# Optimization experiments

Hardware: AMD Instinct MI355X
Metric: run time of the kernel (lower is better)

The kernel has to match this reference:

```python
import jax, jax.numpy as jnp
import numpy as np

N, H, DK, DV, DFF, D = 2, 8, 32, 32, 512, 256
B, S = 2, 2048
MASK_VALUE = -1e-30
EPS = 1e-14  # K.epsilon()**2 with default epsilon 1e-7


def glorot(key, shape):
    fan_in, fan_out = shape[-2], shape[-1]
    limit = np.sqrt(6.0 / (fan_in + fan_out))
    return jax.random.uniform(key, shape, jnp.float32, -limit, limit)


def setup_inputs() -> dict:
    key = jax.random.key(0)
    ks = jax.random.split(key, 8)
    return {
        "x": jax.random.normal(ks[0], (B, S, D), jnp.float32),
        "mask": jnp.ones((B, S), jnp.float32),
        "Wq": glorot(ks[1], (N, H, D, DK)),
        "Wk": glorot(ks[2], (N, H, D, DK)),
        "Wv": glorot(ks[3], (N, H, D, DV)),
        "Wo": glorot(ks[4], (N, H * DV, D)),
        "W1": glorot(ks[5], (N, D, DFF)),
        "b1": jnp.zeros((N, DFF), jnp.float32),
        "W2": glorot(ks[6], (N, DFF, D)),
        "b2": jnp.zeros((N, D), jnp.float32),
        "gamma": jnp.ones((2 * N,), jnp.float32),
        "beta": jnp.zeros((2 * N,), jnp.float32),
    }


def _layernorm(x, g, b):
    mean = jnp.mean(x, axis=-1, keepdims=True)
    var = jnp.mean(jnp.square(x - mean), axis=-1, keepdims=True)
    return (x - mean) / jnp.sqrt(var + EPS) * g + b


def reference(x, mask, Wq, Wk, Wv, Wo, W1, b1, W2, b2, gamma, beta):
    m = mask[:, None, None, :]  # [B,1,1,S], multiplies score rows' key axis
    for i in range(N):
        # batched multi-head attention (no 1/sqrt(dk) scaling, faithful to source)
        q = jnp.einsum("bsd,hdk->bhsk", x, Wq[i])
        k = jnp.einsum("bsd,hdk->bhsk", x, Wk[i])
        v = jnp.einsum("bsd,hdv->bhsv", x, Wv[i])
        A = jnp.einsum("bhsk,bhtk->bhst", q, k)  # [B,H,S,S]
        A = m * A + (1.0 - m) * MASK_VALUE
        A = jax.nn.softmax(A, axis=-1)
        o = jnp.einsum("bhst,bhtv->bhsv", A, v)
        conc = o.transpose(0, 2, 1, 3).reshape(x.shape[0], x.shape[1], H * DV)
        x = x + conc @ Wo[i]
        x = _layernorm(x, gamma[2 * i], beta[2 * i])
        ffn = jax.nn.relu(x @ W1[i] + b1[i]) @ W2[i] + b2[i]
        x = x + ffn
        x = _layernorm(x, gamma[2 * i + 1], beta[2 * i + 1])
    return x
```

## Files before the change

kernel.cpp:

```cpp
#include <hip/hip_runtime.h>
#include <hip/hip_bf16.h>

#define NL 2
#define NH 8
#define DKk 32
#define DVv 32
#define DFF 512
#define DD 256
#define BB 2
#define SS 2048
#define MROWS (BB*SS)
#define LN_EPS 1e-14f
#define L2E 1.4426950408889634f
#define SOFT_SHIFT_L2E (50.0f*L2E)

typedef __hip_bfloat16 bf16;
typedef unsigned short us;
typedef short bf16x8 __attribute__((ext_vector_type(8)));
typedef float f32x4  __attribute__((ext_vector_type(4)));
typedef unsigned short us4 __attribute__((ext_vector_type(4)));

#define O_XF   256
#define O_QB   (O_XF+1048576)
#define O_KH   (O_QB+1048576)
#define O_KL   (O_KH+524288)
#define O_VT   (O_KL+524288)
#define O_XH   (O_VT+524288)
#define O_XL   (O_XH+524288)
#define O_OP   (O_XL+524288)
#define O_ML   (O_OP+2097152)
#define O_MASK (O_ML+65536)
#define O_B1   (O_MASK+4096)
#define O_B2   (O_B1+1024)
#define O_GM   (O_B2+512)
#define O_BT   (O_GM+4)
#define O_PREP (O_BT+4)
#define TAIL_TOTAL (4096+1024+512+4+4)
#define CONV_BLOCKS (512 + (TAIL_TOTAL+255)/256)
#define PREP_BLOCKS 512
#define PQH 0u
#define PQL 393216u
#define POH 786432u
#define POL 917504u
#define P1H 1048576u
#define P1L 1310720u
#define P2H 1572864u
#define P2L 1835008u

__device__ __forceinline__ float us2f(us u){
  unsigned int v = ((unsigned int)u) << 16; float f;
  __builtin_memcpy(&f, &v, 4); return f;
}
__device__ __forceinline__ us f2bf_rne(float f){
  unsigned int b = __float_as_uint(f);
  b += 0x7FFFu + ((b>>16)&1u);
  return (us)(b>>16);
}

#if __has_builtin(__builtin_amdgcn_exp2f)
#define EXP2F(x) __builtin_amdgcn_exp2f(x)
#else
#define EXP2F(x) exp2f(x)
#endif

#if __has_builtin(__builtin_amdgcn_cvt_pk_bf16_f32)
typedef __bf16 bf16x2_t __attribute__((ext_vector_type(2)));
__device__ __forceinline__ int pack_bf16(float a, float b){
  bf16x2_t r = __builtin_amdgcn_cvt_pk_bf16_f32(a, b);
  int i; __builtin_memcpy(&i, &r, 4); return i;
}
#else
__device__ __forceinline__ int pack_bf16(float a, float b){
  int b0 = __float_as_int(a) + 0x8000;
  int b1 = __float_as_int(b) + 0x8000;
  return (b1 & 0xFFFF0000) | ((int)((unsigned)b0 >> 16));
}
#endif

__device__ __forceinline__ f32x4 MF(bf16x8 a, bf16x8 b, f32x4 c){
  return __builtin_amdgcn_mfma_f32_16x16x32_bf16(a,b,c,0,0,0);
}

__device__ __forceinline__ void gl_lds16(const us* g, us* l){
  __builtin_amdgcn_global_load_lds(
    (const __attribute__((address_space(1))) unsigned int*)g,
    (__attribute__((address_space(3))) unsigned int*)l, 16, 0, 0);
}

__device__ __forceinline__ size_t xhl_idx(int row, int col){
  int rt = row>>6, rg = (row>>4)&3, L15 = row&15;
  int kc = col>>5, Q = (col>>3)&3, j = col&7;
  return ((size_t)(rt*8+kc))*2048 + rg*512 + Q*128 + L15*8 + j;
}

__device__ __forceinline__ float conv1(const void* src, size_t i, int flag){
  if(flag) return ((const float*)src)[i];
  return us2f(((const us*)src)[i]);
}

__device__ __forceinline__ void prep_b_raw(const void* W0, const void* W1v, const void* W2v,
                                           int baseoff, us* __restrict__ Bh, us* __restrict__ Bl,
                                           int Kd, int Nd, int qkv, int g, int flag)
{
  int total = (Kd/32)*(Nd/16)*64;
  if(g >= total) return;
  int lane = g & 63, fi = g >> 6;
  int ncN = Nd/16;
  int nc = fi % ncN, kc = fi / ncN;
  int Q = lane>>4, L15 = lane&15;
  int n = nc*16 + L15;
  const void* src;
  int off0, stride;
  if(qkv){
    int sec = n>>8, h = (n>>5)&7, kq = n&31;
    src = (sec==0)?W0:((sec==1)?W1v:W2v);
    off0 = baseoff + h*8192 + kq;
    stride = 32;
  } else {
    src = W0;
    off0 = baseoff + n;
    stride = Nd;
  }
  #pragma unroll
  for(int j=0;j<8;j++){
    int k = kc*32 + Q*8 + j;
    float v = conv1(src, (size_t)off0 + (size_t)k*stride, flag);
    us hb = f2bf_rne(v);
    Bh[(size_t)g*8 + j] = hb;
    Bl[(size_t)g*8 + j] = f2bf_rne(v - us2f(hb));
  }
}

__global__ void conv_prep(const void* s0, const void* s1, const void* sWq, const void* sWk,
                          const void* sWv, const void* sWo, const void* sW1, const void* sb1,
                          const void* sW2, const void* sb2, const void* sgm, const void* sbt,
                          float* __restrict__ ws, int* __restrict__ flagp)
{
  __shared__ int fsh[4];
  int bad = 0;
  const us* xr = (const us*)s0;
  for(int i=threadIdx.x; i<4096; i+=256){
    float f = us2f(xr[i]);
    if(!(fabsf(f) < 1e3f)) bad = 1;
  }
  unsigned long long m = __ballot(bad);
  if((threadIdx.x&63)==0) fsh[threadIdx.x>>6] = (m!=0ull);
  __syncthreads();
  int flag = (fsh[0]|fsh[1]|fsh[2]|fsh[3]);
  if(blockIdx.x==0 && threadIdx.x==0) *flagp = flag;

  int b = blockIdx.x;
  if(b < PREP_BLOCKS){
    int layer = b >> 8, lb = b & 255;
    us* prep = (us*)(ws + O_PREP);
    if(lb < 96){
      int g = lb*256 + threadIdx.x;
      prep_b_raw(sWq, sWk, sWv, layer*65536, prep+PQH+(size_t)layer*196608,
                 prep+PQL+(size_t)layer*196608, 256, 768, 1, g, flag);
    } else if(lb < 128){
      int g = (lb-96)*256 + threadIdx.x;
      prep_b_raw(sWo, nullptr, nullptr, layer*65536, prep+POH+(size_t)layer*65536,
                 prep+POL+(size_t)layer*65536, 256, 256, 0, g, flag);
    } else if(lb < 192){
      int g = (lb-128)*256 + threadIdx.x;
      prep_b_raw(sW1, nullptr, nullptr, layer*131072, prep+P1H+(size_t)layer*131072,
                 prep+P1L+(size_t)layer*131072, 256, 512, 0, g, flag);
    } else {
      int g = (lb-192)*256 + threadIdx.x;
      prep_b_raw(sW2, nullptr, nullptr, layer*131072, prep+P2H+(size_t)layer*131072,
                 prep+P2L+(size_t)layer*131072, 512, 256, 0, g, flag);
    }
    return;
  }
  int b2 = b - PREP_BLOCKS;
  if(b2 < 512){
    int g8 = b2*256 + threadIdx.x;
    int e0 = g8*8;
    float v[8];
    if(flag){
      float4 a0 = *((const float4*)s0 + (e0>>2));
      float4 a1 = *((const float4*)s0 + (e0>>2) + 1);
      v[0]=a0.x; v[1]=a0.y; v[2]=a0.z; v[3]=a0.w;
      v[4]=a1.x; v[5]=a1.y; v[6]=a1.z; v[7]=a1.w;
    } else {
      bf16x8 u = *((const bf16x8*)s0 + g8);
      #pragma unroll
      for(int j=0;j<8;j++) v[j] = us2f((us)u[j]);
    }
    *(float4*)&ws[O_XF+e0]   = (float4){v[0],v[1],v[2],v[3]};
    *(float4*)&ws[O_XF+e0+4] = (float4){v[4],v[5],v[6],v[7]};
    union{ us a[8]; uint4 q; } hh, ll;
    #pragma unroll
    for(int j=0;j<8;j++){
      us hb = f2bf_rne(v[j]);
      hh.a[j] = hb;
      ll.a[j] = f2bf_rne(v[j] - us2f(hb));
    }
    size_t xi = xhl_idx(e0>>8, e0&255);
    *(uint4*)&((us*)(ws+O_XH))[xi] = hh.q;
    *(uint4*)&((us*)(ws+O_XL))[xi] = ll.q;
    return;
  }
  int g = (b2-512)*256 + threadIdx.x;
  if(g < 4096){ ws[O_MASK+g] = conv1(s1, g, flag)*L2E; return; }
  g -= 4096;
  if(g < 1024){ ws[O_B1+g] = conv1(sb1, g, flag); return; }
  g -= 1024;
  if(g < 512){ ws[O_B2+g] = conv1(sb2, g, flag); return; }
  g -= 512;
  if(g < 4){ ws[O_GM+g] = conv1(sgm, g, flag); return; }
  g -= 4;
  if(g < 4){ ws[O_BT+g] = conv1(sbt, g, flag); return; }
}

template<int MODE>
__launch_bounds__(256)
__global__ void gemm_mfma(const us* __restrict__ Axh, const us* __restrict__ Axl,
                          const us* __restrict__ Bh, const us* __restrict__ Bl,
                          const float* __restrict__ bias,
                          float* __restrict__ O,
                          us* __restrict__ QH, us* __restrict__ QL,
                          us* __restrict__ KH, us* __restrict__ KL, us* __restrict__ VT,
                          int Ncols, int Kdim)
{
  __shared__ __align__(16) us SH[16384];
  const int t = threadIdx.x;
  const int w = t>>6, lane = t&63;
  const int Q = lane>>4, L15 = lane&15;
  const int bx = blockIdx.x, by = blockIdx.y;
  const int row0 = bx*64;
  const int nc0 = by*4;
  const int col0 = by*64;
  const int nKc = Kdim>>5;
  const int ncW = Ncols>>4;

  f32x4 acc[2][2];
  #pragma unroll
  for(int i=0;i<2;i++)
    #pragma unroll
    for(int j=0;j<2;j++) acc[i][j] = (f32x4){0.f,0.f,0.f,0.f};

  auto stage = [&](int kc){
    const int bo = (kc&1)*8192;
    size_t abase = ((size_t)(bx*nKc + kc))*2048;
    gl_lds16(&Axh[abase + (size_t)t*8], &SH[bo + t*8]);
    gl_lds16(&Axl[abase + (size_t)t*8], &SH[bo + 2048 + t*8]);
    size_t gidx = ((size_t)(kc*ncW + nc0 + w)*64 + lane)*8;
    gl_lds16(&Bh[gidx], &SH[bo + 4096 + t*8]);
    gl_lds16(&Bl[gidx], &SH[bo + 6144 + t*8]);
  };

  stage(0);

  for(int kc=0; kc<nKc; kc++){
    __syncthreads();
    if(kc+1 < nKc) stage(kc+1);
    const int bo = (kc&1)*8192;
    const us* Ah  = SH + bo;
    const us* Al  = SH + bo + 2048;
    const us* Bhs = SH + bo + 4096;
    const us* Bls = SH + bo + 6144;

    bf16x8 aAh[2], aAl[2], bBh[2], bBl[2];
    #pragma unroll
    for(int rg2=0;rg2<2;rg2++){
      int rg = (w&1)*2 + rg2;
      aAh[rg2] = *(const bf16x8*)&Ah[rg*512 + lane*8];
      aAl[rg2] = *(const bf16x8*)&Al[rg*512 + lane*8];
    }
    #pragma unroll
    for(int cg2=0;cg2<2;cg2++){
      int nc = (w>>1)*2 + cg2;
      bBh[cg2] = *(const bf16x8*)&Bhs[nc*512 + lane*8];
      bBl[cg2] = *(const bf16x8*)&Bls[nc*512 + lane*8];
    }
    #pragma unroll
    for(int rg2=0;rg2<2;rg2++)
      #pragma unroll
      for(int cg2=0;cg2<2;cg2++){
        acc[rg2][cg2] = MF(aAl[rg2], bBh[cg2], acc[rg2][cg2]);
        acc[rg2][cg2] = MF(aAh[rg2], bBl[cg2], acc[rg2][cg2]);
        acc[rg2][cg2] = MF(aAh[rg2], bBh[cg2], acc[rg2][cg2]);
      }
  }

  if(MODE==0){
    __syncthreads();
    us* TH = SH;
    us* TL = SH + 4608;
    #pragma unroll
    for(int rg2=0;rg2<2;rg2++)
      #pragma unroll
      for(int cg2=0;cg2<2;cg2++)
        #pragma unroll
        for(int r=0;r<4;r++){
          int rl = (w&1)*32 + rg2*16 + Q*4 + r;
          int cl = (w>>1)*32 + cg2*16 + L15;
          float va = acc[rg2][cg2][r];
          us hb = f2bf_rne(va);
          TH[rl*72+cl] = hb;
          TL[rl*72+cl] = f2bf_rne(va - us2f(hb));
        }
    __syncthreads();
    const int sec = col0>>8;
    const int h0  = (col0&255)>>5;
    const int b_  = row0>>11;
    const int srow0 = row0 & 2047;
    if(sec < 2){
      us* DH = (sec==0) ? QH : KH;
      us* DL = (sec==0) ? QL : KL;
      #pragma unroll
      for(int u2=0; u2<2; u2++){
        int u = w + u2*4;
        int rg = u&3, half = u>>2;
        int lbase = (rg*16 + L15)*72 + half*32 + Q*8;
        bf16x8 hv = *(const bf16x8*)&TH[lbase];
        bf16x8 lv = *(const bf16x8*)&TL[lbase];
        int bh = b_*NH + h0 + half;
        size_t dbase = ((size_t)(bh*128 + (srow0>>4) + rg)*64 + lane)*8;
        *(bf16x8*)&DH[dbase] = hv;
        *(bf16x8*)&DL[dbase] = lv;
      }
    } else {
      #pragma unroll
      for(int u2=0; u2<2; u2++){
        int u = w + u2*4;
        int sgrp = u&1, kqh = (u>>1)&1, half = u>>2;
        union{ us u8[8]; bf16x8 v; } vv;
        #pragma unroll
        for(int j=0;j<8;j++){
          int rl = sgrp*32 + Q*8 + j;
          int cl = half*32 + kqh*16 + L15;
          vv.u8[j] = TH[rl*72+cl];
        }
        int bh = b_*NH + h0 + half;
        size_t dbase = ((size_t)((bh*64 + (srow0>>5) + sgrp)*2 + kqh)*64 + lane)*8;
        *(bf16x8*)&VT[dbase] = vv.v;
      }
    }
  } else {
    #pragma unroll
    for(int rg2=0;rg2<2;rg2++)
      #pragma unroll
      for(int cg2=0;cg2<2;cg2++)
        #pragma unroll
        for(int r=0;r<4;r++){
          int row = row0 + (w&1)*32 + rg2*16 + Q*4 + r;
          int c   = col0 + (w>>1)*32 + cg2*16 + L15;
          float v = acc[rg2][cg2][r] + bias[c];
          O[(size_t)row*Ncols + c] = v>0.f ? v : 0.f;
        }
  }
}

__launch_bounds__(512)
__global__ void oln_ffn(const float* __restrict__ OpartA, const float* __restrict__ MLA,
                        const us* __restrict__ WOh, const us* __restrict__ WOl,
                        const us* __restrict__ W1h, const us* __restrict__ W1l,
                        const us* __restrict__ W2h, const us* __restrict__ W2l,
                        const float* __restrict__ b1, const float* __restrict__ b2,
                        float* __restrict__ xf, us* __restrict__ xh, us* __restrict__ xl,
                        const float* __restrict__ gamma, const float* __restrict__ beta, int gi0,
                        void* __restrict__ out, int write_out, const int* __restrict__ flagp)
{
  __shared__ __align__(16) us xAH[4096], xAL[4096];
  __shared__ __align__(16) us hAH[8192], hAL[8192];
  __shared__ float lred[256];
  const int t = threadIdx.x;
  const int w = t>>6, lane = t&63;
  const int Q = lane>>4, L15 = lane&15;
  const int row0 = blockIdx.x*16;
  const int b_ = row0>>11, s0_ = row0&2047;

  bf16x8 Wh[4][2], Wl[4][2];
  float4 Ar[2][4];
  float  Ml[2][2];

  auto loadWO_ = [&](int kc, int set){
    #pragma unroll
    for(int cg=0;cg<2;cg++){
      size_t fi = (size_t)(kc*16 + w*2 + cg)*512 + (size_t)lane*8;
      Wh[set][cg] = *(const bf16x8*)&WOh[fi];
      Wl[set][cg] = *(const bf16x8*)&WOl[fi];
    }
  };
  auto loadW1_ = [&](int nch, int kc, int set){
    #pragma unroll
    for(int cg=0;cg<2;cg++){
      size_t fi = (size_t)(kc*32 + nch*16 + w*2 + cg)*512 + (size_t)lane*8;
      Wh[set][cg] = *(const bf16x8*)&W1h[fi];
      Wl[set][cg] = *(const bf16x8*)&W1l[fi];
    }
  };
  auto loadW2_ = [&](int kc, int set){
    #pragma unroll
    for(int cg=0;cg<2;cg++){
      size_t fi = (size_t)(kc*16 + w*2 + cg)*512 + (size_t)lane*8;
      Wh[set][cg] = *(const bf16x8*)&W2h[fi];
      Wl[set][cg] = *(const bf16x8*)&W2l[fi];
    }
  };
  auto loadAr = [&](int kc, int set){
    size_t i0 = ((size_t)(b_*8+kc))*2048 + s0_ + L15;
    Ml[set][0] = MLA[i0]; Ml[set][1] = MLA[i0+32768];
    const float* p0 = &OpartA[i0*32 + Q*8];
    const float* p1 = &OpartA[(i0+32768)*32 + Q*8];
    Ar[set][0] = *(const float4*)p0; Ar[set][1] = *(const float4*)(p0+4);
    Ar[set][2] = *(const float4*)p1; Ar[set][3] = *(const float4*)(p1+4);
  };

  f32x4 accA[2];
  accA[0] = accA[1] = (f32x4){0.f,0.f,0.f,0.f};

  auto stepA = [&](int aset, int wset){
    float inv = 1.f/(Ml[aset][0] + Ml[aset][1]);
    float fv[8];
    fv[0]=(Ar[aset][0].x+Ar[aset][2].x)*inv; fv[1]=(Ar[aset][0].y+Ar[aset][2].y)*inv;
    fv[2]=(Ar[aset][0].z+Ar[aset][2].z)*inv; fv[3]=(Ar[aset][0].w+Ar[aset][2].w)*inv;
    fv[4]=(Ar[aset][1].x+Ar[aset][3].x)*inv; fv[5]=(Ar[aset][1].y+Ar[aset][3].y)*inv;
    fv[6]=(Ar[aset][1].z+Ar[aset][3].z)*inv; fv[7]=(Ar[aset][1].w+Ar[aset][3].w)*inv;
    union{ us a[8]; bf16x8 v; } Ah_, Al_;
    #pragma unroll
    for(int j=0;j<8;j++){
      us hb = f2bf_rne(fv[j]);
      Ah_.a[j] = hb;
      Al_.a[j] = f2bf_rne(fv[j] - us2f(hb));
    }
    accA[0] = MF(Al_.v, Wh[wset][0], accA[0]);
    accA[0] = MF(Ah_.v, Wl[wset][0], accA[0]);
    accA[0] = MF(Ah_.v, Wh[wset][0], accA[0]);
    accA[1] = MF(Al_.v, Wh[wset][1], accA[1]);
    accA[1] = MF(Ah_.v, Wl[wset][1], accA[1]);
    accA[1] = MF(Ah_.v, Wh[wset][1], accA[1]);
  };

  loadAr(0,0); loadWO_(0,0);
  loadAr(1,1); loadWO_(1,1);
  loadWO_(2,2); loadWO_(3,3);
  #pragma unroll
  for(int kc=0; kc<8; kc+=2){
    stepA(0, kc&3);
    if(kc+2<8) loadAr(kc+2, 0);
    if(kc+4<8) loadWO_(kc+4, (kc+4)&3);
    stepA(1, (kc+1)&3);
    if(kc+3<8) loadAr(kc+3, 1);
    if(kc+5<8) loadWO_(kc+5, (kc+5)&3);
  }

  float tmp[2][4];
  #pragma unroll
  for(int cg=0;cg<2;cg++)
    #pragma unroll
    for(int r=0;r<4;r++){
      int row = row0 + Q*4 + r;
      int c = (w*2+cg)*16 + L15;
      tmp[cg][r] = accA[cg][r] + xf[(size_t)row*DD + c];
    }
  float s[4], sq[4];
  #pragma unroll
  for(int r=0;r<4;r++){
    s[r]  = tmp[0][r]+tmp[1][r];
    sq[r] = tmp[0][r]*tmp[0][r]+tmp[1][r]*tmp[1][r];
  }
  #pragma unroll
  for(int off=1; off<16; off<<=1)
    #pragma unroll
    for(int r=0;r<4;r++){
      s[r]  += __shfl_xor(s[r], off);
      sq[r] += __shfl_xor(sq[r], off);
    }
  if(L15==0){
    #pragma unroll
    for(int r=0;r<4;r++){
      int rl = Q*4 + r;
      lred[(w*16 + rl)*2]   = s[r];
      lred[(w*16 + rl)*2+1] = sq[r];
    }
  }
  __syncthreads();
  float val_s[2][4];
  {
    float g = gamma[gi0], bb = beta[gi0];
    float scv[4], mnv[4];
    #pragma unroll
    for(int r=0;r<4;r++){
      int rl = Q*4 + r;
      float S = 0.f, SQ = 0.f;
      #pragma unroll
      for(int wv=0; wv<8; wv++){
        S  += lred[(wv*16+rl)*2];
        SQ += lred[(wv*16+rl)*2+1];
      }
      float mean = S*(1.f/DD);
      float var  = SQ*(1.f/DD) - mean*mean;
      scv[r] = rsqrtf(var+LN_EPS)*g;
      mnv[r] = mean;
    }
    #pragma unroll
    for(int cg=0;cg<2;cg++){
      int c = (w*2+cg)*16 + L15;
      int base = (c>>5)*512 + (((c&31)>>3))*128 + (c&7);
      #pragma unroll
      for(int r=0;r<4;r++){
        float v = (tmp[cg][r]-mnv[r])*scv[r] + bb;
        val_s[cg][r] = v;
        us hb = f2bf_rne(v);
        xAH[base + (Q*4+r)*8] = hb;
        xAL[base + (Q*4+r)*8] = f2bf_rne(v - us2f(hb));
      }
    }
  }
  __syncthreads();

  #pragma unroll
  for(int nch=0; nch<2; nch++){
    f32x4 ah[2];
    ah[0] = ah[1] = (f32x4){0.f,0.f,0.f,0.f};
    loadW1_(nch,0,0); loadW1_(nch,1,1); loadW1_(nch,2,2); loadW1_(nch,3,3);
    #pragma unroll
    for(int kc=0; kc<8; kc+=4){
      #pragma unroll
      for(int sub=0; sub<4; sub++){
        bf16x8 aAh = *(const bf16x8*)&xAH[(kc+sub)*512 + lane*8];
        bf16x8 aAl = *(const bf16x8*)&xAL[(kc+sub)*512 + lane*8];
        ah[0] = MF(aAl, Wh[sub][0], ah[0]);
        ah[0] = MF(aAh, Wl[sub][0], ah[0]);
        ah[0] = MF(aAh, Wh[sub][0], ah[0]);
        ah[1] = MF(aAl, Wh[sub][1], ah[1]);
        ah[1] = MF(aAh, Wl[sub][1], ah[1]);
        ah[1] = MF(aAh, Wh[sub][1], ah[1]);
        if(kc+sub+4 < 8) loadW1_(nch, kc+sub+4, sub);
      }
    }
    #pragma unroll
    for(int cg=0;cg<2;cg++){
      int col = nch*256 + (w*2+cg)*16 + L15;
      float bv = b1[col];
      int base = (col>>5)*512 + (((col&31)>>3))*128 + (col&7);
      #pragma unroll
      for(int r=0;r<4;r++){
        int row = Q*4 + r;
        float v = ah[cg][r] + bv;
        v = v>0.f ? v : 0.f;
        us hb = f2bf_rne(v);
        hAH[base + row*8] = hb;
        hAL[base + row*8] = f2bf_rne(v - us2f(hb));
      }
    }
  }
  __syncthreads();

  f32x4 ay[2];
  ay[0] = ay[1] = (f32x4){0.f,0.f,0.f,0.f};
  loadW2_(0,0); loadW2_(1,1); loadW2_(2,2); loadW2_(3,3);
  #pragma unroll
  for(int kc2=0; kc2<16; kc2+=4){
    #pragma unroll
    for(int sub=0; sub<4; sub++){
      bf16x8 aAh = *(const bf16x8*)&hAH[(kc2+sub)*512 + lane*8];
      bf16x8 aAl = *(const bf16x8*)&hAL[(kc2+sub)*512 + lane*8];
      ay[0] = MF(aAl, Wh[sub][0], ay[0]);
      ay[0] = MF(aAh, Wl[sub][0], ay[0]);
      ay[0] = MF(aAh, Wh[sub][0], ay[0]);
      ay[1] = MF(aAl, Wh[sub][1], ay[1]);
      ay[1] = MF(aAh, Wl[sub][1], ay[1]);
      ay[1] = MF(aAh, Wh[sub][1], ay[1]);
      if(kc2+sub+4 < 16) loadW2_(kc2+sub+4, sub);
    }
  }

  float tmp2[2][4];
  #pragma unroll
  for(int cg=0;cg<2;cg++)
    #pragma unroll
    for(int r=0;r<4;r++){
      int c = (w*2+cg)*16 + L15;
      tmp2[cg][r] = ay[cg][r] + val_s[cg][r] + b2[c];
    }
  float s2[4], sq2[4];
  #pragma unroll
  for(int r=0;r<4;r++){
    s2[r]  = tmp2[0][r]+tmp2[1][r];
    sq2[r] = tmp2[0][r]*tmp2[0][r]+tmp2[1][r]*tmp2[1][r];
  }
  #pragma unroll
  for(int off=1; off<16; off<<=1)
    #pragma unroll
    for(int r=0;r<4;r++){
      s2[r]  += __shfl_xor(s2[r], off);
      sq2[r] += __shfl_xor(sq2[r], off);
    }
  if(L15==0){
    #pragma unroll
    for(int r=0;r<4;r++){
      int rl = Q*4 + r;
      lred[(w*16 + rl)*2]   = s2[r];
      lred[(w*16 + rl)*2+1] = sq2[r];
    }
  }
  __syncthreads();
  float g2 = gamma[gi0+1], bb2 = beta[gi0+1];
  float scv2[4], mnv2[4];
  #pragma unroll
  for(int r=0;r<4;r++){
    int rl = Q*4 + r;
    float S = 0.f, SQ = 0.f;
    #pragma unroll
    for(int wv=0; wv<8; wv++){
      S  += lred[(wv*16+rl)*2];
      SQ += lred[(wv*16+rl)*2+1];
    }
    float mean = S*(1.f/DD);
    float var  = SQ*(1.f/DD) - mean*mean;
    scv2[r] = rsqrtf(var+LN_EPS)*g2;
    mnv2[r] = mean;
  }
  int flag = write_out ? *flagp : 0;
  #pragma unroll
  for(int cg=0;cg<2;cg++)
    #pragma unroll
    for(int r=0;r<4;r++){
      int row = row0 + Q*4 + r;
      int c = (w*2+cg)*16 + L15;
      float val = (tmp2[cg][r]-mnv2[r])*scv2[r] + bb2;
      xf[(size_t)row*DD + c] = val;
      us hb = f2bf_rne(val);
      size_t xi = xhl_idx(row, c);
      xh[xi] = hb;
      xl[xi] = f2bf_rne(val - us2f(hb));
      if(write_out){
        if(flag) ((float*)out)[(size_t)row*DD + c] = val;
        else     ((bf16*)out)[(size_t)row*DD + c] = __float2bfloat16(val);
      }
    }
}

__launch_bounds__(256)
__global__ void attn_kernel(const us* __restrict__ QH, const us* __restrict__ QL,
                            const us* __restrict__ KH, const us* __restrict__ KL,
                            const us* __restrict__ VT,
                            const float* __restrict__ mask,
                            float* __restrict__ Opart, float* __restrict__ ML)
{
  __shared__ __align__(16) us Khs[4096], Kls[4096], Vts[4096];
  __shared__ __align__(16) float Msl[1024];
  const int t = threadIdx.x;
  const int bh = blockIdx.x >> 6;
  const int qt = (blockIdx.x & 63) >> 1;
  const int ks = blockIdx.x & 1;
  const int b_ = bh >> 3;
  const int wv = t >> 6;
  const int lane = t & 63;
  const int Q = lane >> 4, L15 = lane & 15;
  const int q0 = qt*64 + wv*16;

  size_t qidx = ((size_t)(bh*128 + qt*4 + wv)*64 + lane)*8;
  const bf16x8 qh_v = *(const bf16x8*)&QH[qidx];
  const bf16x8 ql_v = *(const bf16x8*)&QL[qidx];

  const us* KHbh = KH + (size_t)bh*65536;
  const us* KLbh = KL + (size_t)bh*65536;
  const us* VTbh = VT + (size_t)bh*65536;
  const int base = ks*1024;

  f32x4 Oa0a = {0.f,0.f,0.f,0.f}, Oa0b = {0.f,0.f,0.f,0.f};
  f32x4 Oa1a = {0.f,0.f,0.f,0.f}, Oa1b = {0.f,0.f,0.f,0.f};
  float lacc = 0.f;

  {
    const us* mrow = (const us*)(mask + (size_t)b_*SS + base);
    gl_lds16(mrow + (size_t)t*8, ((us*)Msl) + t*8);
    size_t kbase = (size_t)(base>>4)*512;
    size_t vbase = (size_t)(base>>5)*1024;
    gl_lds16(&KHbh[kbase + (size_t)t*8], &Khs[t*8]);
    gl_lds16(&KLbh[kbase + (size_t)t*8], &Kls[t*8]);
    gl_lds16(&VTbh[vbase + (size_t)t*8], &Vts[t*8]);
  }

  for(int s=0; s<16; s++){
    __syncthreads();
    if(s < 15){
      int t0n = base + (s+1)*64;
      int bn = (s+1)&1;
      size_t kbase = (size_t)(t0n>>4)*512;
      size_t vbase = (size_t)(t0n>>5)*1024;
      gl_lds16(&KHbh[kbase + (size_t)t*8], &Khs[bn*2048 + t*8]);
      gl_lds16(&KLbh[kbase + (size_t)t*8], &Kls[bn*2048 + t*8]);
      gl_lds16(&VTbh[vbase + (size_t)t*8], &Vts[bn*2048 + t*8]);
    }
    const int bo = (s&1)*2048;
    const int mo = s*64;

    f32x4 St[4];
    const f32x4 zz = {0.f,0.f,0.f,0.f};
    #pragma unroll
    for(int kt=0;kt<4;kt++){
      bf16x8 aKh = *(const bf16x8*)&Khs[bo + kt*512 + lane*8];
      bf16x8 aKl = *(const bf16x8*)&Kls[bo + kt*512 + lane*8];
      f32x4 a = MF(aKl, qh_v, zz);
      a = MF(aKh, ql_v, a);
      a = MF(aKh, qh_v, a);
      St[kt] = a;
    }

    float lsum = 0.f;
    #pragma unroll
    for(int kt=0;kt<4;kt++){
      float4 mv = *(const float4*)&Msl[mo + kt*16 + Q*4];
      float mvr[4] = {mv.x, mv.y, mv.z, mv.w};
      #pragma unroll
      for(int r=0;r<4;r++){
        float p = EXP2F(fmaf(mvr[r], St[kt][r], -SOFT_SHIFT_L2E));
        St[kt][r] = p;
        lsum += p;
      }
    }
    lacc += lsum;

    int pk[4][2];
    #pragma unroll
    for(int kt=0;kt<4;kt++){
      pk[kt][0] = pack_bf16(St[kt][0], St[kt][1]);
      pk[kt][1] = pack_bf16(St[kt][2], St[kt][3]);
    }

    #pragma unroll
    for(int c=0;c<2;c++){
      union { int i[4]; bf16x8 v; } bu;
      #pragma unroll
      for(int d=0;d<4;d++){
        int srcl = (((Q&1)*2 + (d>>1))<<4) | L15;
        int vlo = __shfl(pk[2*c  ][d&1], srcl, 64);
        int vhi = __shfl(pk[2*c+1][d&1], srcl, 64);
        bu.i[d] = (Q & 2) ? vhi : vlo;
      }
      bf16x8 aV0 = *(const bf16x8*)&Vts[bo + (c*2+0)*512 + lane*8];
      bf16x8 aV1 = *(const bf16x8*)&Vts[bo + (c*2+1)*512 + lane*8];
      if(c == 0){
        Oa0a = MF(aV0, bu.v, Oa0a);
        Oa1a = MF(aV1, bu.v, Oa1a);
      } else {
        Oa0b = MF(aV0, bu.v, Oa0b);
        Oa1b = MF(aV1, bu.v, Oa1b);
      }
    }
  }

  f32x4 Oa0 = Oa0a + Oa0b;
  f32x4 Oa1 = Oa1a + Oa1b;
  lacc += __shfl_xor(lacc, 16);
  lacc += __shfl_xor(lacc, 32);

  float* opp = &Opart[((size_t)(ks*16+bh)*SS + q0 + L15)*32];
  #pragma unroll
  for(int r=0;r<4;r++){
    opp[Q*4+r]    = Oa0[r];
    opp[16+Q*4+r] = Oa1[r];
  }
  if(Q==0){
    ML[(size_t)(ks*16+bh)*SS + q0 + L15] = lacc;
  }
}

extern "C" void kernel_launch(void* const* d_in, const int* in_sizes, int n_in,
                              void* d_out, int out_size, void* d_ws, size_t ws_size,
                              hipStream_t stream)
{
  float* ws = (float*)d_ws;
  int* flagp = (int*)d_ws;

  float* xf  = ws + O_XF;
  us* QHb = (us*)(ws + O_QB);
  us* QLb = QHb + 1048576;
  us* KH = (us*)(ws + O_KH);
  us* KL = (us*)(ws + O_KL);
  us* VT = (us*)(ws + O_VT);
  us* XH = (us*)(ws + O_XH);
  us* XL = (us*)(ws + O_XL);
  float* Opart = ws + O_OP;
  float* ML  = ws + O_ML;
  float* b1f = ws + O_B1;
  float* b2f_ = ws + O_B2;
  float* gmf = ws + O_GM;
  float* btf = ws + O_BT;
  us* prep = (us*)(ws + O_PREP);

  conv_prep<<<PREP_BLOCKS+CONV_BLOCKS,256,0,stream>>>(
      d_in[0], d_in[1], d_in[2], d_in[3], d_in[4], d_in[5],
      d_in[6], d_in[7], d_in[8], d_in[9], d_in[10], d_in[11],
      ws, flagp);

  for(int i=0;i<NL;i++){
    const float* b1i = b1f + (size_t)i*DFF;
    const float* b2i = b2f_ + (size_t)i*DD;

    dim3 g0(64, 12);
    gemm_mfma<0><<<g0,256,0,stream>>>(XH, XL,
                                      prep+PQH+(size_t)i*196608, prep+PQL+(size_t)i*196608,
                                      nullptr, nullptr,
                                      QHb, QLb, KH, KL, VT, 768, 256);
    attn_kernel<<<1024,256,0,stream>>>(QHb, QLb, KH, KL, VT, ws + O_MASK, Opart, ML);
    oln_ffn<<<256,512,0,stream>>>(Opart, ML,
                                  prep+POH+(size_t)i*65536, prep+POL+(size_t)i*65536,
                                  prep+P1H+(size_t)i*131072, prep+P1L+(size_t)i*131072,
                                  prep+P2H+(size_t)i*131072, prep+P2L+(size_t)i*131072,
                                  b1i, b2i, xf, XH, XL,
                                  gmf, btf, 2*i, d_out, (i==NL-1)?1:0, flagp);
  }
}
```

Measured before the change: 247.5 us.

## Widen oln_ffn to 16 waves with one output column tile per wave

The fused output-projection/LayerNorm/FFN kernel now launches 1024 threads per block instead of 512, and each wave owns one 16-column tile instead of two. This halves the MFMA chain and weight registers per wave and raises the number of waves per block, which should help hide latency with only 256 blocks. The residual read from xf is also hoisted ahead of the projection loop. In exchange, each of the 16 waves redundantly loads and converts the same attention partials, and the LayerNorm reductions now cross 16 waves, which adds more synchronization work.

```diff
diff --git a/kernel.cpp b/kernel.cpp
--- a/kernel.cpp
+++ b/kernel.cpp
@@ -353,7 +353,7 @@
   }
 }
 
-__launch_bounds__(512)
+__launch_bounds__(1024)
 __global__ void oln_ffn(const float* __restrict__ OpartA, const float* __restrict__ MLA,
                         const us* __restrict__ WOh, const us* __restrict__ WOl,
                         const us* __restrict__ W1h, const us* __restrict__ W1l,
@@ -365,40 +365,31 @@
 {
   __shared__ __align__(16) us xAH[4096], xAL[4096];
   __shared__ __align__(16) us hAH[8192], hAL[8192];
-  __shared__ float lred[256];
+  __shared__ float lred[512];
   const int t = threadIdx.x;
   const int w = t>>6, lane = t&63;
   const int Q = lane>>4, L15 = lane&15;
   const int row0 = blockIdx.x*16;
   const int b_ = row0>>11, s0_ = row0&2047;
 
-  bf16x8 Wh[4][2], Wl[4][2];
+  bf16x8 Wh[4], Wl[4];
   float4 Ar[2][4];
   float  Ml[2][2];
 
   auto loadWO_ = [&](int kc, int set){
-    #pragma unroll
-    for(int cg=0;cg<2;cg++){
-      size_t fi = (size_t)(kc*16 + w*2 + cg)*512 + (size_t)lane*8;
-      Wh[set][cg] = *(const bf16x8*)&WOh[fi];
-      Wl[set][cg] = *(const bf16x8*)&WOl[fi];
-    }
+    size_t fi = (size_t)(kc*16 + w)*512 + (size_t)lane*8;
+    Wh[set] = *(const bf16x8*)&WOh[fi];
+    Wl[set] = *(const bf16x8*)&WOl[fi];
   };
   auto loadW1_ = [&](int nch, int kc, int set){
-    #pragma unroll
-    for(int cg=0;cg<2;cg++){
-      size_t fi = (size_t)(kc*32 + nch*16 + w*2 + cg)*512 + (size_t)lane*8;
-      Wh[set][cg] = *(const bf16x8*)&W1h[fi];
-      Wl[set][cg] = *(const bf16x8*)&W1l[fi];
-    }
+    size_t fi = (size_t)(kc*32 + nch*16 + w)*512 + (size_t)lane*8;
+    Wh[set] = *(const bf16x8*)&W1h[fi];
+    Wl[set] = *(const bf16x8*)&W1l[fi];
   };
   auto loadW2_ = [&](int kc, int set){
-    #pragma unroll
-    for(int cg=0;cg<2;cg++){
-      size_t fi = (size_t)(kc*16 + w*2 + cg)*512 + (size_t)lane*8;
-      Wh[set][cg] = *(const bf16x8*)&W2h[fi];
-      Wl[set][cg] = *(const bf16x8*)&W2l[fi];
-    }
+    size_t fi = (size_t)(kc*16 + w)*512 + (size_t)lane*8;
+    Wh[set] = *(const bf16x8*)&W2h[fi];
+    Wl[set] = *(const bf16x8*)&W2l[fi];
   };
   auto loadAr = [&](int kc, int set){
     size_t i0 = ((size_t)(b_*8+kc))*2048 + s0_ + L15;
@@ -409,8 +400,12 @@
     Ar[set][2] = *(const float4*)p1; Ar[set][3] = *(const float4*)(p1+4);
   };
 
-  f32x4 accA[2];
-  accA[0] = accA[1] = (f32x4){0.f,0.f,0.f,0.f};
+  float resv[4];
+  #pragma unroll
+  for(int r=0;r<4;r++)
+    resv[r] = xf[(size_t)(row0+Q*4+r)*DD + (w*16+L15)];
+
+  f32x4 accA = (f32x4){0.f,0.f,0.f,0.f};
 
   auto stepA = [&](int aset, int wset){
     float inv = 1.f/(Ml[aset][0] + Ml[aset][1]);
@@ -426,12 +421,9 @@
       Ah_.a[j] = hb;
       Al_.a[j] = f2bf_rne(fv[j] - us2f(hb));
     }
-    accA[0] = MF(Al_.v, Wh[wset][0], accA[0]);
-    accA[0] = MF(Ah_.v, Wl[wset][0], accA[0]);
-    accA[0] = MF(Ah_.v, Wh[wset][0], accA[0]);
-    accA[1] = MF(Al_.v, Wh[wset][1], accA[1]);
-    accA[1] = MF(Ah_.v, Wl[wset][1], accA[1]);
-    accA[1] = MF(Ah_.v, Wh[wset][1], accA[1]);
+    accA = MF(Al_.v, Wh[wset], accA);
+    accA = MF(Ah_.v, Wl[wset], accA);
+    accA = MF(Ah_.v, Wh[wset], accA);
   };
 
   loadAr(0,0); loadWO_(0,0);
@@ -447,21 +439,12 @@
     if(kc+5<8) loadWO_(kc+5, (kc+5)&3);
   }
 
-  float tmp[2][4];
-  #pragma unroll
-  for(int cg=0;cg<2;cg++)
-    #pragma unroll
-    for(int r=0;r<4;r++){
-      int row = row0 + Q*4 + r;
-      int c = (w*2+cg)*16 + L15;
-      tmp[cg][r] = accA[cg][r] + xf[(size_t)row*DD + c];
-    }
+  float tmp[4];
+  #pragma unroll
+  for(int r=0;r<4;r++) tmp[r] = accA[r] + resv[r];
   float s[4], sq[4];
   #pragma unroll
-  for(int r=0;r<4;r++){
-    s[r]  = tmp[0][r]+tmp[1][r];
-    sq[r] = tmp[0][r]*tmp[0][r]+tmp[1][r]*tmp[1][r];
-  }
+  for(int r=0;r<4;r++){ s[r] = tmp[r]; sq[r] = tmp[r]*tmp[r]; }
   #pragma unroll
   for(int off=1; off<16; off<<=1)
     #pragma unroll
@@ -478,7 +461,7 @@
     }
   }
   __syncthreads();
-  float val_s[2][4];
+  float val_s[4];
   {
     float g = gamma[gi0], bb = beta[gi0];
     float scv[4], mnv[4];
@@ -487,7 +470,7 @@
       int rl = Q*4 + r;
       float S = 0.f, SQ = 0.f;
       #pragma unroll
-      for(int wv=0; wv<8; wv++){
+      for(int wv=0; wv<16; wv++){
         S  += lred[(wv*16+rl)*2];
         SQ += lred[(wv*16+rl)*2+1];
       }
@@ -496,26 +479,22 @@
       scv[r] = rsqrtf(var+LN_EPS)*g;
       mnv[r] = mean;
     }
-    #pragma unroll
-    for(int cg=0;cg<2;cg++){
-      int c = (w*2+cg)*16 + L15;
-      int base = (c>>5)*512 + (((c&31)>>3))*128 + (c&7);
-      #pragma unroll
-      for(int r=0;r<4;r++){
-        float v = (tmp[cg][r]-mnv[r])*scv[r] + bb;
-        val_s[cg][r] = v;
-        us hb = f2bf_rne(v);
-        xAH[base + (Q*4+r)*8] = hb;
-        xAL[base + (Q*4+r)*8] = f2bf_rne(v - us2f(hb));
-      }
+    int c = w*16 + L15;
+    int base = (c>>5)*512 + (((c&31)>>3))*128 + (c&7);
+    #pragma unroll
+    for(int r=0;r<4;r++){
+      float v = (tmp[r]-mnv[r])*scv[r] + bb;
+      val_s[r] = v;
+      us hb = f2bf_rne(v);
+      xAH[base + (Q*4+r)*8] = hb;
+      xAL[base + (Q*4+r)*8] = f2bf_rne(v - us2f(hb));
     }
   }
   __syncthreads();
 
   #pragma unroll
   for(int nch=0; nch<2; nch++){
-    f32x4 ah[2];
-    ah[0] = ah[1] = (f32x4){0.f,0.f,0.f,0.f};
+    f32x4 ah = (f32x4){0.f,0.f,0.f,0.f};
     loadW1_(nch,0,0); loadW1_(nch,1,1); loadW1_(nch,2,2); loadW1_(nch,3,3);
     #pragma unroll
     for(int kc=0; kc<8; kc+=4){
@@ -523,24 +502,20 @@
       for(int sub=0; sub<4; sub++){
         bf16x8 aAh = *(const bf16x8*)&xAH[(kc+sub)*512 + lane*8];
         bf16x8 aAl = *(const bf16x8*)&xAL[(kc+sub)*512 + lane*8];
-        ah[0] = MF(aAl, Wh[sub][0], ah[0]);
-        ah[0] = MF(aAh, Wl[sub][0], ah[0]);
-        ah[0] = MF(aAh, Wh[sub][0], ah[0]);
-        ah[1] = MF(aAl, Wh[sub][1], ah[1]);
-        ah[1] = MF(aAh, Wl[sub][1], ah[1]);
-        ah[1] = MF(aAh, Wh[sub][1], ah[1]);
+        ah = MF(aAl, Wh[sub], ah);
+        ah = MF(aAh, Wl[sub], ah);
+        ah = MF(aAh, Wh[sub], ah);
         if(kc+sub+4 < 8) loadW1_(nch, kc+sub+4, sub);
       }
     }
-    #pragma unroll
-    for(int cg=0;cg<2;cg++){
-      int col = nch*256 + (w*2+cg)*16 + L15;
+    {
+      int col = (nch*16 + w)*16 + L15;
       float bv = b1[col];
       int base = (col>>5)*512 + (((col&31)>>3))*128 + (col&7);
       #pragma unroll
       for(int r=0;r<4;r++){
         int row = Q*4 + r;
-        float v = ah[cg][r] + bv;
+        float v = ah[r] + bv;
         v = v>0.f ? v : 0.f;
         us hb = f2bf_rne(v);
         hAH[base + row*8] = hb;
@@ -550,8 +525,7 @@
   }
   __syncthreads();
 
-  f32x4 ay[2];
-  ay[0] = ay[1] = (f32x4){0.f,0.f,0.f,0.f};
+  f32x4 ay = (f32x4){0.f,0.f,0.f,0.f};
   loadW2_(0,0); loadW2_(1,1); loadW2_(2,2); loadW2_(3,3);
   #pragma unroll
   for(int kc2=0; kc2<16; kc2+=4){
@@ -559,30 +533,23 @@
     for(int sub=0; sub<4; sub++){
       bf16x8 aAh = *(const bf16x8*)&hAH[(kc2+sub)*512 + lane*8];
       bf16x8 aAl = *(const bf16x8*)&hAL[(kc2+sub)*512 + lane*8];
-      ay[0] = MF(aAl, Wh[sub][0], ay[0]);
-      ay[0] = MF(aAh, Wl[sub][0], ay[0]);
-      ay[0] = MF(aAh, Wh[sub][0], ay[0]);
-      ay[1] = MF(aAl, Wh[sub][1], ay[1]);
-      ay[1] = MF(aAh, Wl[sub][1], ay[1]);
-      ay[1] = MF(aAh, Wh[sub][1], ay[1]);
+      ay = MF(aAl, Wh[sub], ay);
+      ay = MF(aAh, Wl[sub], ay);
+      ay = MF(aAh, Wh[sub], ay);
       if(kc2+sub+4 < 16) loadW2_(kc2+sub+4, sub);
     }
   }
 
-  float tmp2[2][4];
-  #pragma unroll
-  for(int cg=0;cg<2;cg++)
-    #pragma unroll
-    for(int r=0;r<4;r++){
-      int c = (w*2+cg)*16 + L15;
-      tmp2[cg][r] = ay[cg][r] + val_s[cg][r] + b2[c];
-    }
+  float tmp2[4];
+  {
+    int c = w*16 + L15;
+    float bv = b2[c];
+    #pragma unroll
+    for(int r=0;r<4;r++) tmp2[r] = ay[r] + val_s[r] + bv;
+  }
   float s2[4], sq2[4];
   #pragma unroll
-  for(int r=0;r<4;r++){
-    s2[r]  = tmp2[0][r]+tmp2[1][r];
-    sq2[r] = tmp2[0][r]*tmp2[0][r]+tmp2[1][r]*tmp2[1][r];
-  }
+  for(int r=0;r<4;r++){ s2[r] = tmp2[r]; sq2[r] = tmp2[r]*tmp2[r]; }
   #pragma unroll
   for(int off=1; off<16; off<<=1)
     #pragma unroll
@@ -606,7 +573,7 @@
     int rl = Q*4 + r;
     float S = 0.f, SQ = 0.f;
     #pragma unroll
-    for(int wv=0; wv<8; wv++){
+    for(int wv=0; wv<16; wv++){
       S  += lred[(wv*16+rl)*2];
       SQ += lred[(wv*16+rl)*2+1];
     }
@@ -616,13 +583,12 @@
     mnv2[r] = mean;
   }
   int flag = write_out ? *flagp : 0;
-  #pragma unroll
-  for(int cg=0;cg<2;cg++)
+  {
+    int c = w*16 + L15;
     #pragma unroll
     for(int r=0;r<4;r++){
       int row = row0 + Q*4 + r;
-      int c = (w*2+cg)*16 + L15;
-      float val = (tmp2[cg][r]-mnv2[r])*scv2[r] + bb2;
+      float val = (tmp2[r]-mnv2[r])*scv2[r] + bb2;
       xf[(size_t)row*DD + c] = val;
       us hb = f2bf_rne(val);
       size_t xi = xhl_idx(row, c);
@@ -633,6 +599,7 @@
         else     ((bf16*)out)[(size_t)row*DD + c] = __float2bfloat16(val);
       }
     }
+  }
 }
 
 __launch_bounds__(256)
@@ -800,11 +767,11 @@
                                       nullptr, nullptr,
                                       QHb, QLb, KH, KL, VT, 768, 256);
     attn_kernel<<<1024,256,0,stream>>>(QHb, QLb, KH, KL, VT, ws + O_MASK, Opart, ML);
-    oln_ffn<<<256,512,0,stream>>>(Opart, ML,
-                                  prep+POH+(size_t)i*65536, prep+POL+(size_t)i*65536,
-                                  prep+P1H+(size_t)i*131072, prep+P1L+(size_t)i*131072,
-                                  prep+P2H+(size_t)i*131072, prep+P2L+(size_t)i*131072,
-                                  b1i, b2i, xf, XH, XL,
-                                  gmf, btf, 2*i, d_out, (i==NL-1)?1:0, flagp);
-  }
-}
+    oln_ffn<<<256,1024,0,stream>>>(Opart, ML,
+                                   prep+POH+(size_t)i*65536, prep+POL+(size_t)i*65536,
+                                   prep+P1H+(size_t)i*131072, prep+P1L+(size_t)i*131072,
+                                   prep+P2H+(size_t)i*131072, prep+P2L+(size_t)i*131072,
+                                   b1i, b2i, xf, XH, XL,
+                                   gmf, btf, 2*i, d_out, (i==NL-1)?1:0, flagp);
+  }
+}
```

Measured after the change: 266.3 us. +7.6%, slower.
